# Kernel tuning notes

Hardware: AMD Instinct MI355X
Metric: run time of the kernel (lower is better)

## Reference

```python
import jax, jax.numpy as jnp
import numpy as np

D = 128
N_SRC = 50000
N_DST = 50000
E = 640000
NEG_SLOPE = 0.01  # torch LeakyReLU default


def _lrelu(x):
    return jax.nn.leaky_relu(x, NEG_SLOPE)


def setup_inputs() -> dict:
    key = jax.random.key(0)
    ks = jax.random.split(key, 12)
    s = 1.0 / np.sqrt(D)
    return {
        "feat_src": jax.random.normal(ks[0], (N_SRC, D), jnp.float32),
        "feat_dst": jax.random.normal(ks[1], (N_DST, D), jnp.float32),
        "src_idx": jax.random.randint(ks[2], (E,), 0, N_SRC, jnp.int32),
        "dst_idx": jax.random.randint(ks[3], (E,), 0, N_DST, jnp.int32),
        "W_src": jax.random.uniform(ks[4], (D, D), jnp.float32, -s, s),
        "b_src": jnp.zeros((D,), jnp.float32),
        "W_dst": jax.random.uniform(ks[5], (D, D), jnp.float32, -s, s),
        "b_dst": jnp.zeros((D,), jnp.float32),
        "W_a1": jax.random.uniform(ks[6], (D, D), jnp.float32, -s, s),
        "b_a1": jnp.zeros((D,), jnp.float32),
        "W_a2": jax.random.uniform(ks[7], (D, 1), jnp.float32, -s, s),
        "b_a2": jnp.zeros((1,), jnp.float32),
        "W_out": jax.random.uniform(ks[8], (D, D), jnp.float32, -s, s),
        "b_out": jnp.zeros((D,), jnp.float32),
    }


def reference(feat_src, feat_dst, src_idx, dst_idx,
              W_src, b_src, W_dst, b_dst,
              W_a1, b_a1, W_a2, b_a2, W_out, b_out):
    n_dst = feat_dst.shape[0]
    # node projections (dropout is identity in eval mode)
    hs = feat_src @ W_src + b_src            # [n_src, d]
    hd = feat_dst @ W_dst + b_dst            # [n_dst, d]
    # u_add_v: per-edge feature
    e = hs[src_idx] + hd[dst_idx]            # [E, d]
    # attention MLP: LeakyReLU -> Linear -> LeakyReLU -> Linear(d->1)
    s = _lrelu(_lrelu(e) @ W_a1 + b_a1) @ W_a2 + b_a2  # [E, 1]
    s = s[:, 0]
    # edge softmax grouped by destination node (numerically stable)
    m = jax.ops.segment_max(s, dst_idx, num_segments=n_dst)
    ex = jnp.exp(s - m[dst_idx])
    denom = jax.ops.segment_sum(ex, dst_idx, num_segments=n_dst)
    alpha = ex / denom[dst_idx]              # [E]
    # scale messages and scatter-sum to dst nodes
    n_f = jax.ops.segment_sum(alpha[:, None] * e, dst_idx, num_segments=n_dst)
    return _lrelu(n_f @ W_out + b_out)       # [n_dst, d]
```

## Files before the change

kernel.cpp:

```cpp
#include <hip/hip_runtime.h>
#include <math.h>

#define DD 128
#define NEG 0.01f
#define SCHUNK 4096

typedef __attribute__((ext_vector_type(8))) _Float16 half8;
typedef __attribute__((ext_vector_type(4))) float f32x4;

__device__ __forceinline__ float lrelu(float x){ return x > 0.f ? x : NEG * x; }

__device__ __forceinline__ unsigned short h2u(_Float16 h){
    union { _Float16 h; unsigned short u; } v; v.h = h; return v.u;
}
__device__ __forceinline__ _Float16 u2h(unsigned short u){
    union { unsigned short u; _Float16 h; } v; v.u = u; return v.h;
}

__global__ void hist_pack(const int* dst, int* deg, int E, int nhist,
                          const float* Wa1, const float* Wsrc,
                          const float* Wdst, const float* Wout,
                          unsigned short* wpack){
    const int bid = blockIdx.x;
    if (bid < nhist){
        int i = bid * 256 + threadIdx.x;
        if (i < E) atomicAdd(&deg[dst[i]], 1);
    } else {
        int i = (bid - nhist) * 256 + threadIdx.x;
        if (i >= 7 * 16384) return;
        int seg = i >> 14, t = i & 16383;
        int j = t & 7, lane = (t >> 3) & 63, nt = (t >> 9) & 7, kc = t >> 12;
        int k = kc * 32 + (lane >> 4) * 8 + j;
        int n = nt * 16 + (lane & 15);
        const float* W = (seg == 0) ? Wa1 : (seg <= 2) ? Wsrc : (seg <= 4) ? Wdst : Wout;
        float w = W[k * DD + n];
        _Float16 hi = (_Float16)w;
        unsigned short val = h2u(hi);
        if (seg == 2 || seg == 4 || seg == 6) val = h2u((_Float16)(w - (float)hi));
        wpack[i] = val;
    }
}

__global__ __launch_bounds__(1024) void scan1(const int* deg, int* part, int n){
    __shared__ int wsum[16];
    const int tid = threadIdx.x;
    const int lane = tid & 63, wid = tid >> 6;
    int i4 = blockIdx.x * SCHUNK + tid * 4;
    int4 v = make_int4(0, 0, 0, 0);
    if (i4 + 3 < n) v = *(const int4*)(deg + i4);
    else {
        if (i4 + 0 < n) v.x = deg[i4 + 0];
        if (i4 + 1 < n) v.y = deg[i4 + 1];
        if (i4 + 2 < n) v.z = deg[i4 + 2];
        if (i4 + 3 < n) v.w = deg[i4 + 3];
    }
    int t = v.x + v.y + v.z + v.w;
    #pragma unroll
    for (int off = 1; off < 64; off <<= 1) t += __shfl_xor(t, off, 64);
    if (lane == 0) wsum[wid] = t;
    __syncthreads();
    if (tid == 0){
        int s = 0;
        #pragma unroll
        for (int j = 0; j < 16; j++) s += wsum[j];
        part[blockIdx.x] = s;
    }
}

__global__ __launch_bounds__(1024) void scan2(const int* deg, const int* part,
        int* row_off, int* cursor, int n, int nchunks){
    __shared__ int wsum[16];
    const int tid = threadIdx.x;
    const int lane = tid & 63, wid = tid >> 6;
    const int b = blockIdx.x;
    int carry = 0;
    for (int j = 0; j < b; j++) carry += part[j];
    int i4 = b * SCHUNK + tid * 4;
    int4 v = make_int4(0, 0, 0, 0);
    if (i4 + 3 < n) v = *(const int4*)(deg + i4);
    else {
        if (i4 + 0 < n) v.x = deg[i4 + 0];
        if (i4 + 1 < n) v.y = deg[i4 + 1];
        if (i4 + 2 < n) v.z = deg[i4 + 2];
        if (i4 + 3 < n) v.w = deg[i4 + 3];
    }
    int tsum = v.x + v.y + v.z + v.w;
    int x = tsum;
    #pragma unroll
    for (int off = 1; off < 64; off <<= 1){
        int t = __shfl_up(x, off, 64);
        if (lane >= off) x += t;
    }
    if (lane == 63) wsum[wid] = x;
    __syncthreads();
    int wprefix = 0;
    #pragma unroll
    for (int j = 0; j < 16; j++) if (j < wid) wprefix += wsum[j];
    int excl = carry + wprefix + (x - tsum);
    if (i4 + 3 < n){
        int4 o;
        o.x = excl; o.y = excl + v.x; o.z = o.y + v.y; o.w = o.z + v.z;
        *(int4*)(row_off + i4) = o;
        *(int4*)(cursor + i4) = o;
    } else {
        int a = excl;
        if (i4 + 0 < n){ row_off[i4 + 0] = a; cursor[i4 + 0] = a; a += v.x; }
        if (i4 + 1 < n){ row_off[i4 + 1] = a; cursor[i4 + 1] = a; a += v.y; }
        if (i4 + 2 < n){ row_off[i4 + 2] = a; cursor[i4 + 2] = a; a += v.z; }
        if (i4 + 3 < n){ row_off[i4 + 3] = a; cursor[i4 + 3] = a; }
    }
    if (b == 0 && tid == 0){
        int tot = 0;
        for (int j = 0; j < nchunks; j++) tot += part[j];
        row_off[n] = tot;
    }
}

__global__ void scatter_pairs(const int* src, const int* dst, int* cursor,
                              int2* pairs, int* s_srcs, int E){
    int i = blockIdx.x * blockDim.x + threadIdx.x;
    if (i < E){
        int d = dst[i];
        int s = src[i];
        int pos = atomicAdd(&cursor[d], 1);
        pairs[pos] = make_int2(s, d);
        s_srcs[pos] = s;
    }
}

__global__ __launch_bounds__(256) void lin2_mfma(
        const float* X1, const unsigned short* W1hi, const unsigned short* W1lo,
        const float* b1, unsigned short* Yb1, int n1, int g1,
        const float* X2, const unsigned short* W2hi, const unsigned short* W2lo,
        const float* b2, unsigned short* Yb2, int n2){
    __shared__ unsigned short sB[2][16384];
    const int tid = threadIdx.x;
    const int second = (blockIdx.x >= g1);
    const float* X = second ? X2 : X1;
    const unsigned short* Whi = second ? W2hi : W1hi;
    const unsigned short* Wlo = second ? W2lo : W1lo;
    const float* b = second ? b2 : b1;
    unsigned short* Yb = second ? Yb2 : Yb1;
    const int nrows = second ? n2 : n1;
    const int bidx = second ? (blockIdx.x - g1) : blockIdx.x;
    {
        const uint4* gh = (const uint4*)Whi;
        const uint4* gl = (const uint4*)Wlo;
        uint4* lh = (uint4*)sB[0];
        uint4* ll = (uint4*)sB[1];
        #pragma unroll
        for (int t = 0; t < 8; t++){
            lh[tid + 256 * t] = gh[tid + 256 * t];
            ll[tid + 256 * t] = gl[tid + 256 * t];
        }
    }
    const int wave = tid >> 6, lane = tid & 63;
    const int qd = lane >> 4, ln16 = lane & 15;
    const int row0 = bidx * 128 + wave * 32;
    int r0 = row0 + ln16;       if (r0 >= nrows) r0 = nrows - 1;
    int r1 = row0 + 16 + ln16;  if (r1 >= nrows) r1 = nrows - 1;
    f32x4 acc[2][8];
    #pragma unroll
    for (int rt = 0; rt < 2; rt++)
        #pragma unroll
        for (int nt = 0; nt < 8; nt++)
            acc[rt][nt] = (f32x4){0.f, 0.f, 0.f, 0.f};
    __syncthreads();
    #pragma unroll
    for (int kc = 0; kc < 4; kc++){
        const int koff = kc * 32 + qd * 8;
        half8 ahi[2], alo[2];
        const float* px[2] = {X + (size_t)r0 * DD + koff, X + (size_t)r1 * DD + koff};
        #pragma unroll
        for (int rt = 0; rt < 2; rt++){
            float4 v0 = *(const float4*)(px[rt]);
            float4 v1 = *(const float4*)(px[rt] + 4);
            float xv[8] = {v0.x, v0.y, v0.z, v0.w, v1.x, v1.y, v1.z, v1.w};
            #pragma unroll
            for (int j = 0; j < 8; j++){
                _Float16 h = (_Float16)xv[j];
                ahi[rt][j] = h;
                alo[rt][j] = (_Float16)(xv[j] - (float)h);
            }
        }
        #pragma unroll
        for (int nt = 0; nt < 8; nt++){
            const int fi = (((kc << 3) + nt) << 6 | lane) << 3;
            half8 bh = *(const half8*)&sB[0][fi];
            half8 bl = *(const half8*)&sB[1][fi];
            #pragma unroll
            for (int rt = 0; rt < 2; rt++){
                acc[rt][nt] = __builtin_amdgcn_mfma_f32_16x16x32_f16(ahi[rt], bh, acc[rt][nt], 0, 0, 0);
                acc[rt][nt] = __builtin_amdgcn_mfma_f32_16x16x32_f16(alo[rt], bh, acc[rt][nt], 0, 0, 0);
                acc[rt][nt] = __builtin_amdgcn_mfma_f32_16x16x32_f16(ahi[rt], bl, acc[rt][nt], 0, 0, 0);
            }
        }
    }
    #pragma unroll
    for (int nt = 0; nt < 8; nt++){
        const int col = nt * 16 + ln16;
        const float bv = b[col];
        #pragma unroll
        for (int rt = 0; rt < 2; rt++){
            #pragma unroll
            for (int r = 0; r < 4; r++){
                int row = row0 + rt * 16 + qd * 4 + r;
                if (row < nrows){
                    float y = acc[rt][nt][r] + bv;
                    Yb[(size_t)row * DD + col] = h2u((_Float16)y);
                }
            }
        }
    }
}

__global__ __launch_bounds__(256) void lin_mfma(const float* X,
        const unsigned short* Whi, const unsigned short* Wlo, const float* b,
        float* Y, int nrows){
    __shared__ unsigned short sB[2][16384];
    const int tid = threadIdx.x;
    {
        const uint4* gh = (const uint4*)Whi;
        const uint4* gl = (const uint4*)Wlo;
        uint4* lh = (uint4*)sB[0];
        uint4* ll = (uint4*)sB[1];
        #pragma unroll
        for (int t = 0; t < 8; t++){
            lh[tid + 256 * t] = gh[tid + 256 * t];
            ll[tid + 256 * t] = gl[tid + 256 * t];
        }
    }
    const int wave = tid >> 6, lane = tid & 63;
    const int qd = lane >> 4, ln16 = lane & 15;
    const int row0 = blockIdx.x * 128 + wave * 32;
    int r0 = row0 + ln16;       if (r0 >= nrows) r0 = nrows - 1;
    int r1 = row0 + 16 + ln16;  if (r1 >= nrows) r1 = nrows - 1;
    f32x4 acc[2][8];
    #pragma unroll
    for (int rt = 0; rt < 2; rt++)
        #pragma unroll
        for (int nt = 0; nt < 8; nt++)
            acc[rt][nt] = (f32x4){0.f, 0.f, 0.f, 0.f};
    __syncthreads();
    #pragma unroll
    for (int kc = 0; kc < 4; kc++){
        const int koff = kc * 32 + qd * 8;
        half8 ahi[2], alo[2];
        const float* px[2] = {X + (size_t)r0 * DD + koff, X + (size_t)r1 * DD + koff};
        #pragma unroll
        for (int rt = 0; rt < 2; rt++){
            float4 v0 = *(const float4*)(px[rt]);
            float4 v1 = *(const float4*)(px[rt] + 4);
            float xv[8] = {v0.x, v0.y, v0.z, v0.w, v1.x, v1.y, v1.z, v1.w};
            #pragma unroll
            for (int j = 0; j < 8; j++){
                _Float16 h = (_Float16)xv[j];
                ahi[rt][j] = h;
                alo[rt][j] = (_Float16)(xv[j] - (float)h);
            }
        }
        #pragma unroll
        for (int nt = 0; nt < 8; nt++){
            const int fi = (((kc << 3) + nt) << 6 | lane) << 3;
            half8 bh = *(const half8*)&sB[0][fi];
            half8 bl = *(const half8*)&sB[1][fi];
            #pragma unroll
            for (int rt = 0; rt < 2; rt++){
                acc[rt][nt] = __builtin_amdgcn_mfma_f32_16x16x32_f16(ahi[rt], bh, acc[rt][nt], 0, 0, 0);
                acc[rt][nt] = __builtin_amdgcn_mfma_f32_16x16x32_f16(alo[rt], bh, acc[rt][nt], 0, 0, 0);
                acc[rt][nt] = __builtin_amdgcn_mfma_f32_16x16x32_f16(ahi[rt], bl, acc[rt][nt], 0, 0, 0);
            }
        }
    }
    #pragma unroll
    for (int nt = 0; nt < 8; nt++){
        const int col = nt * 16 + ln16;
        const float bv = b[col];
        #pragma unroll
        for (int rt = 0; rt < 2; rt++){
            #pragma unroll
            for (int r = 0; r < 4; r++){
                int row = row0 + rt * 16 + qd * 4 + r;
                if (row < nrows){
                    float y = acc[rt][nt][r] + bv;
                    Y[(size_t)row * DD + col] = lrelu(y);
                }
            }
        }
    }
}

__device__ __forceinline__ half8 make_afrag(const unsigned short* ph, const unsigned short* pd){
    half8 a = *(const half8*)ph;
    half8 b = *(const half8*)pd;
    half8 s = a + b;
    half8 l = s * (_Float16)0.01f;
    half8 r;
    #pragma unroll
    for (int i = 0; i < 8; i++) r[i] = (s[i] > (_Float16)0.f) ? s[i] : l[i];
    return r;
}

__global__ __launch_bounds__(256) void edge_score_mfma(
        const unsigned short* hs_h, const unsigned short* hd_h,
        const int2* pairs,
        const unsigned short* wa1p, const float* ba1,
        const float* Wa2, const float* ba2,
        float* s_w, int E){
    __shared__ unsigned short sB[16384];
    const int tid = threadIdx.x;
    {
        const uint4* g = (const uint4*)wa1p;
        uint4* l = (uint4*)sB;
        #pragma unroll
        for (int t = 0; t < 8; t++) l[tid + 256 * t] = g[tid + 256 * t];
    }
    const int wave = tid >> 6, lane = tid & 63;
    const int qd = lane >> 4, ln16 = lane & 15;
    float b1v[8], w2v[8];
    #pragma unroll
    for (int nt = 0; nt < 8; nt++){
        b1v[nt] = ba1[nt * 16 + ln16];
        w2v[nt] = Wa2[nt * 16 + ln16];
    }
    const float b2 = ba2[0];
    __syncthreads();
    for (int half = 0; half < 2; half++){
        const int e0 = blockIdx.x * 256 + half * 128 + wave * 32;
        for (int rt = 0; rt < 2; rt++){
            int eid = e0 + rt * 16 + ln16;
            if (eid >= E) eid = E - 1;
            const int2 pp = pairs[eid];
            f32x4 acc[8];
            #pragma unroll
            for (int nt = 0; nt < 8; nt++) acc[nt] = (f32x4){0.f, 0.f, 0.f, 0.f};
            #pragma unroll
            for (int kc = 0; kc < 4; kc++){
                const int koff = kc * 32 + qd * 8;
                half8 af = make_afrag(hs_h + (size_t)pp.x * DD + koff,
                                      hd_h + (size_t)pp.y * DD + koff);
                #pragma unroll
                for (int nt = 0; nt < 8; nt++){
                    half8 bf = *(const half8*)&sB[(((kc << 3) + nt) << 6 | lane) << 3];
                    acc[nt] = __builtin_amdgcn_mfma_f32_16x16x32_f16(af, bf, acc[nt], 0, 0, 0);
                }
            }
            float p[4] = {0.f, 0.f, 0.f, 0.f};
            #pragma unroll
            for (int nt = 0; nt < 8; nt++)
                #pragma unroll
                for (int r = 0; r < 4; r++){
                    float z = acc[nt][r] + b1v[nt];
                    z = z > 0.f ? z : NEG * z;
                    p[r] += z * w2v[nt];
                }
            #pragma unroll
            for (int r = 0; r < 4; r++){
                float v = p[r];
                #pragma unroll
                for (int off = 1; off < 16; off <<= 1) v += __shfl_xor(v, off, 64);
                p[r] = expf(v + b2);
            }
            if (ln16 == 0){
                int row = e0 + rt * 16 + qd * 4;
                #pragma unroll
                for (int r = 0; r < 4; r++)
                    if (row + r < E) s_w[row + r] = p[r];
            }
        }
    }
}

__global__ __launch_bounds__(256) void agg_softmax(const unsigned short* hs_h,
        const unsigned short* hd_h, const int* row_off, const int* s_srcs,
        const float* s_w, float* nf, int n_dst){
    const int w = (blockIdx.x * blockDim.x + threadIdx.x) >> 6;
    const int lane = threadIdx.x & 63;
    if (w >= n_dst) return;
    const int beg = row_off[w], end = row_off[w + 1];
    float2 acc = make_float2(0.f, 0.f);
    float sa = 0.f;
    int e = beg;
    for (; e + 3 < end; e += 4){
        float w0 = s_w[e], w1 = s_w[e + 1], w2 = s_w[e + 2], w3 = s_w[e + 3];
        int s0 = s_srcs[e], s1 = s_srcs[e + 1], s2 = s_srcs[e + 2], s3 = s_srcs[e + 3];
        ushort2 u0 = *(const ushort2*)(hs_h + (size_t)s0 * DD + lane * 2);
        ushort2 u1 = *(const ushort2*)(hs_h + (size_t)s1 * DD + lane * 2);
        ushort2 u2 = *(const ushort2*)(hs_h + (size_t)s2 * DD + lane * 2);
        ushort2 u3 = *(const ushort2*)(hs_h + (size_t)s3 * DD + lane * 2);
        acc.x += w0 * (float)u2h(u0.x) + w1 * (float)u2h(u1.x)
               + w2 * (float)u2h(u2.x) + w3 * (float)u2h(u3.x);
        acc.y += w0 * (float)u2h(u0.y) + w1 * (float)u2h(u1.y)
               + w2 * (float)u2h(u2.y) + w3 * (float)u2h(u3.y);
        sa += (w0 + w1) + (w2 + w3);
    }
    for (; e < end; e++){
        float w0 = s_w[e];
        int s0 = s_srcs[e];
        ushort2 u0 = *(const ushort2*)(hs_h + (size_t)s0 * DD + lane * 2);
        acc.x += w0 * (float)u2h(u0.x);
        acc.y += w0 * (float)u2h(u0.y);
        sa += w0;
    }
    const float inv = (end > beg) ? 1.f / sa : 0.f;
    ushort2 hu = *(const ushort2*)(hd_h + (size_t)w * DD + lane * 2);
    const float hx = (end > beg) ? (float)u2h(hu.x) : 0.f;
    const float hy = (end > beg) ? (float)u2h(hu.y) : 0.f;
    float2 out;
    out.x = acc.x * inv + hx;
    out.y = acc.y * inv + hy;
    *(float2*)(nf + (size_t)w * DD + lane * 2) = out;
}

extern "C" void kernel_launch(void* const* d_in, const int* in_sizes, int n_in,
                              void* d_out, int out_size, void* d_ws, size_t ws_size,
                              hipStream_t stream){
    const float* feat_src = (const float*)d_in[0];
    const float* feat_dst = (const float*)d_in[1];
    const int*   src_idx  = (const int*)d_in[2];
    const int*   dst_idx  = (const int*)d_in[3];
    const float* W_src = (const float*)d_in[4];
    const float* b_src = (const float*)d_in[5];
    const float* W_dst = (const float*)d_in[6];
    const float* b_dst = (const float*)d_in[7];
    const float* W_a1  = (const float*)d_in[8];
    const float* b_a1  = (const float*)d_in[9];
    const float* W_a2  = (const float*)d_in[10];
    const float* b_a2  = (const float*)d_in[11];
    const float* W_out = (const float*)d_in[12];
    const float* b_out = (const float*)d_in[13];
    const int n_src = in_sizes[0] / DD;
    const int n_dst = in_sizes[1] / DD;
    const int E = in_sizes[2];
    const int nchunks = (n_dst + SCHUNK - 1) / SCHUNK;

    char* p = (char*)d_ws;
    unsigned short* hs_h = (unsigned short*)p;  p += (size_t)n_src * DD * 2;
    unsigned short* hd_h = (unsigned short*)p;  p += (size_t)n_dst * DD * 2;
    unsigned short* wpack = (unsigned short*)p; p += 7 * 16384 * 2;
    float* s_w = (float*)p;                     p += (size_t)E * 4;
    int2* pairs = (int2*)p;                     p += (size_t)E * 8;
    int* s_srcs = (int*)p;                      p += (size_t)E * 4;
    int* deg = (int*)p;                         p += (size_t)n_dst * 4;
    int* cursor = (int*)p;                      p += (size_t)n_dst * 4;
    int* part = (int*)p;                        p += 64 * 4;
    int* row_off = (int*)p;                     p += ((size_t)n_dst + 1) * 4;
    float* nf = (float*)d_out;

    const unsigned short* wa1p    = wpack;
    const unsigned short* wsrc_hi = wpack + 1 * 16384;
    const unsigned short* wsrc_lo = wpack + 2 * 16384;
    const unsigned short* wdst_hi = wpack + 3 * 16384;
    const unsigned short* wdst_lo = wpack + 4 * 16384;
    const unsigned short* wout_hi = wpack + 5 * 16384;
    const unsigned short* wout_lo = wpack + 6 * 16384;

    hipMemsetAsync(deg, 0, (size_t)n_dst * 4, stream);
    const int nhist = (E + 255) / 256;
    const int npack = (7 * 16384 + 255) / 256;
    hist_pack<<<nhist + npack, 256, 0, stream>>>(dst_idx, deg, E, nhist,
                                                 W_a1, W_src, W_dst, W_out, wpack);
    scan1<<<nchunks, 1024, 0, stream>>>(deg, part, n_dst);
    scan2<<<nchunks, 1024, 0, stream>>>(deg, part, row_off, cursor, n_dst, nchunks);
    scatter_pairs<<<(E + 255) / 256, 256, 0, stream>>>(src_idx, dst_idx, cursor,
                                                       pairs, s_srcs, E);
    const int g1 = (n_src + 127) / 128;
    const int g2 = (n_dst + 127) / 128;
    lin2_mfma<<<g1 + g2, 256, 0, stream>>>(feat_src, wsrc_hi, wsrc_lo, b_src, hs_h, n_src, g1,
                                           feat_dst, wdst_hi, wdst_lo, b_dst, hd_h, n_dst);
    edge_score_mfma<<<(E + 255) / 256, 256, 0, stream>>>(hs_h, hd_h, pairs, wa1p, b_a1,
                                                         W_a2, b_a2, s_w, E);
    agg_softmax<<<((size_t)n_dst * 64 + 255) / 256, 256, 0, stream>>>(hs_h, hd_h, row_off,
                                                                      s_srcs, s_w, nf, n_dst);
    lin_mfma<<<g2, 256, 0, stream>>>(nf, wout_hi, wout_lo, b_out, nf, n_dst);
}
```

Before: 325.0 us.

## Drop split-fp16 GEMM compensation, halve edge-score block work, unroll aggregation by 8

```diff
diff --git a/kernel.cpp b/kernel.cpp
--- a/kernel.cpp
+++ b/kernel.cpp
@@ -27,17 +27,13 @@
         if (i < E) atomicAdd(&deg[dst[i]], 1);
     } else {
         int i = (bid - nhist) * 256 + threadIdx.x;
-        if (i >= 7 * 16384) return;
+        if (i >= 4 * 16384) return;
         int seg = i >> 14, t = i & 16383;
         int j = t & 7, lane = (t >> 3) & 63, nt = (t >> 9) & 7, kc = t >> 12;
         int k = kc * 32 + (lane >> 4) * 8 + j;
         int n = nt * 16 + (lane & 15);
-        const float* W = (seg == 0) ? Wa1 : (seg <= 2) ? Wsrc : (seg <= 4) ? Wdst : Wout;
-        float w = W[k * DD + n];
-        _Float16 hi = (_Float16)w;
-        unsigned short val = h2u(hi);
-        if (seg == 2 || seg == 4 || seg == 6) val = h2u((_Float16)(w - (float)hi));
-        wpack[i] = val;
+        const float* W = (seg == 0) ? Wa1 : (seg == 1) ? Wsrc : (seg == 2) ? Wdst : Wout;
+        wpack[i] = h2u((_Float16)W[k * DD + n]);
     }
 }
 
@@ -129,30 +125,24 @@
 }
 
 __global__ __launch_bounds__(256) void lin2_mfma(
-        const float* X1, const unsigned short* W1hi, const unsigned short* W1lo,
-        const float* b1, unsigned short* Yb1, int n1, int g1,
-        const float* X2, const unsigned short* W2hi, const unsigned short* W2lo,
-        const float* b2, unsigned short* Yb2, int n2){
-    __shared__ unsigned short sB[2][16384];
+        const float* X1, const unsigned short* W1, const float* b1,
+        unsigned short* Yb1, int n1, int g1,
+        const float* X2, const unsigned short* W2, const float* b2,
+        unsigned short* Yb2, int n2){
+    __shared__ unsigned short sB[16384];
     const int tid = threadIdx.x;
     const int second = (blockIdx.x >= g1);
     const float* X = second ? X2 : X1;
-    const unsigned short* Whi = second ? W2hi : W1hi;
-    const unsigned short* Wlo = second ? W2lo : W1lo;
+    const unsigned short* W = second ? W2 : W1;
     const float* b = second ? b2 : b1;
     unsigned short* Yb = second ? Yb2 : Yb1;
     const int nrows = second ? n2 : n1;
     const int bidx = second ? (blockIdx.x - g1) : blockIdx.x;
     {
-        const uint4* gh = (const uint4*)Whi;
-        const uint4* gl = (const uint4*)Wlo;
-        uint4* lh = (uint4*)sB[0];
-        uint4* ll = (uint4*)sB[1];
-        #pragma unroll
-        for (int t = 0; t < 8; t++){
-            lh[tid + 256 * t] = gh[tid + 256 * t];
-            ll[tid + 256 * t] = gl[tid + 256 * t];
-        }
+        const uint4* g = (const uint4*)W;
+        uint4* l = (uint4*)sB;
+        #pragma unroll
+        for (int t = 0; t < 8; t++) l[tid + 256 * t] = g[tid + 256 * t];
     }
     const int wave = tid >> 6, lane = tid & 63;
     const int qd = lane >> 4, ln16 = lane & 15;
@@ -169,31 +159,23 @@
     #pragma unroll
     for (int kc = 0; kc < 4; kc++){
         const int koff = kc * 32 + qd * 8;
-        half8 ahi[2], alo[2];
+        half8 a[2];
         const float* px[2] = {X + (size_t)r0 * DD + koff, X + (size_t)r1 * DD + koff};
         #pragma unroll
         for (int rt = 0; rt < 2; rt++){
             float4 v0 = *(const float4*)(px[rt]);
             float4 v1 = *(const float4*)(px[rt] + 4);
-            float xv[8] = {v0.x, v0.y, v0.z, v0.w, v1.x, v1.y, v1.z, v1.w};
-            #pragma unroll
-            for (int j = 0; j < 8; j++){
-                _Float16 h = (_Float16)xv[j];
-                ahi[rt][j] = h;
-                alo[rt][j] = (_Float16)(xv[j] - (float)h);
-            }
+            a[rt][0] = (_Float16)v0.x; a[rt][1] = (_Float16)v0.y;
+            a[rt][2] = (_Float16)v0.z; a[rt][3] = (_Float16)v0.w;
+            a[rt][4] = (_Float16)v1.x; a[rt][5] = (_Float16)v1.y;
+            a[rt][6] = (_Float16)v1.z; a[rt][7] = (_Float16)v1.w;
         }
         #pragma unroll
         for (int nt = 0; nt < 8; nt++){
             const int fi = (((kc << 3) + nt) << 6 | lane) << 3;
-            half8 bh = *(const half8*)&sB[0][fi];
-            half8 bl = *(const half8*)&sB[1][fi];
-            #pragma unroll
-            for (int rt = 0; rt < 2; rt++){
-                acc[rt][nt] = __builtin_amdgcn_mfma_f32_16x16x32_f16(ahi[rt], bh, acc[rt][nt], 0, 0, 0);
-                acc[rt][nt] = __builtin_amdgcn_mfma_f32_16x16x32_f16(alo[rt], bh, acc[rt][nt], 0, 0, 0);
-                acc[rt][nt] = __builtin_amdgcn_mfma_f32_16x16x32_f16(ahi[rt], bl, acc[rt][nt], 0, 0, 0);
-            }
+            half8 bw = *(const half8*)&sB[fi];
+            acc[0][nt] = __builtin_amdgcn_mfma_f32_16x16x32_f16(a[0], bw, acc[0][nt], 0, 0, 0);
+            acc[1][nt] = __builtin_amdgcn_mfma_f32_16x16x32_f16(a[1], bw, acc[1][nt], 0, 0, 0);
         }
     }
     #pragma unroll
@@ -215,20 +197,14 @@
 }
 
 __global__ __launch_bounds__(256) void lin_mfma(const float* X,
-        const unsigned short* Whi, const unsigned short* Wlo, const float* b,
-        float* Y, int nrows){
-    __shared__ unsigned short sB[2][16384];
+        const unsigned short* W, const float* b, float* Y, int nrows){
+    __shared__ unsigned short sB[16384];
     const int tid = threadIdx.x;
     {
-        const uint4* gh = (const uint4*)Whi;
-        const uint4* gl = (const uint4*)Wlo;
-        uint4* lh = (uint4*)sB[0];
-        uint4* ll = (uint4*)sB[1];
-        #pragma unroll
-        for (int t = 0; t < 8; t++){
-            lh[tid + 256 * t] = gh[tid + 256 * t];
-            ll[tid + 256 * t] = gl[tid + 256 * t];
-        }
+        const uint4* g = (const uint4*)W;
+        uint4* l = (uint4*)sB;
+        #pragma unroll
+        for (int t = 0; t < 8; t++) l[tid + 256 * t] = g[tid + 256 * t];
     }
     const int wave = tid >> 6, lane = tid & 63;
     const int qd = lane >> 4, ln16 = lane & 15;
@@ -245,31 +221,23 @@
     #pragma unroll
     for (int kc = 0; kc < 4; kc++){
         const int koff = kc * 32 + qd * 8;
-        half8 ahi[2], alo[2];
+        half8 a[2];
         const float* px[2] = {X + (size_t)r0 * DD + koff, X + (size_t)r1 * DD + koff};
         #pragma unroll
         for (int rt = 0; rt < 2; rt++){
             float4 v0 = *(const float4*)(px[rt]);
             float4 v1 = *(const float4*)(px[rt] + 4);
-            float xv[8] = {v0.x, v0.y, v0.z, v0.w, v1.x, v1.y, v1.z, v1.w};
-            #pragma unroll
-            for (int j = 0; j < 8; j++){
-                _Float16 h = (_Float16)xv[j];
-                ahi[rt][j] = h;
-                alo[rt][j] = (_Float16)(xv[j] - (float)h);
-            }
+            a[rt][0] = (_Float16)v0.x; a[rt][1] = (_Float16)v0.y;
+            a[rt][2] = (_Float16)v0.z; a[rt][3] = (_Float16)v0.w;
+            a[rt][4] = (_Float16)v1.x; a[rt][5] = (_Float16)v1.y;
+            a[rt][6] = (_Float16)v1.z; a[rt][7] = (_Float16)v1.w;
         }
         #pragma unroll
         for (int nt = 0; nt < 8; nt++){
             const int fi = (((kc << 3) + nt) << 6 | lane) << 3;
-            half8 bh = *(const half8*)&sB[0][fi];
-            half8 bl = *(const half8*)&sB[1][fi];
-            #pragma unroll
-            for (int rt = 0; rt < 2; rt++){
-                acc[rt][nt] = __builtin_amdgcn_mfma_f32_16x16x32_f16(ahi[rt], bh, acc[rt][nt], 0, 0, 0);
-                acc[rt][nt] = __builtin_amdgcn_mfma_f32_16x16x32_f16(alo[rt], bh, acc[rt][nt], 0, 0, 0);
-                acc[rt][nt] = __builtin_amdgcn_mfma_f32_16x16x32_f16(ahi[rt], bl, acc[rt][nt], 0, 0, 0);
-            }
+            half8 bw = *(const half8*)&sB[fi];
+            acc[0][nt] = __builtin_amdgcn_mfma_f32_16x16x32_f16(a[0], bw, acc[0][nt], 0, 0, 0);
+            acc[1][nt] = __builtin_amdgcn_mfma_f32_16x16x32_f16(a[1], bw, acc[1][nt], 0, 0, 0);
         }
     }
     #pragma unroll
@@ -317,6 +285,7 @@
     }
     const int wave = tid >> 6, lane = tid & 63;
     const int qd = lane >> 4, ln16 = lane & 15;
+    const int e0 = blockIdx.x * 128 + wave * 32;
     float b1v[8], w2v[8];
     #pragma unroll
     for (int nt = 0; nt < 8; nt++){
@@ -325,48 +294,45 @@
     }
     const float b2 = ba2[0];
     __syncthreads();
-    for (int half = 0; half < 2; half++){
-        const int e0 = blockIdx.x * 256 + half * 128 + wave * 32;
-        for (int rt = 0; rt < 2; rt++){
-            int eid = e0 + rt * 16 + ln16;
-            if (eid >= E) eid = E - 1;
-            const int2 pp = pairs[eid];
-            f32x4 acc[8];
-            #pragma unroll
-            for (int nt = 0; nt < 8; nt++) acc[nt] = (f32x4){0.f, 0.f, 0.f, 0.f};
-            #pragma unroll
-            for (int kc = 0; kc < 4; kc++){
-                const int koff = kc * 32 + qd * 8;
-                half8 af = make_afrag(hs_h + (size_t)pp.x * DD + koff,
-                                      hd_h + (size_t)pp.y * DD + koff);
-                #pragma unroll
-                for (int nt = 0; nt < 8; nt++){
-                    half8 bf = *(const half8*)&sB[(((kc << 3) + nt) << 6 | lane) << 3];
-                    acc[nt] = __builtin_amdgcn_mfma_f32_16x16x32_f16(af, bf, acc[nt], 0, 0, 0);
-                }
+    for (int rt = 0; rt < 2; rt++){
+        int eid = e0 + rt * 16 + ln16;
+        if (eid >= E) eid = E - 1;
+        const int2 pp = pairs[eid];
+        f32x4 acc[8];
+        #pragma unroll
+        for (int nt = 0; nt < 8; nt++) acc[nt] = (f32x4){0.f, 0.f, 0.f, 0.f};
+        #pragma unroll
+        for (int kc = 0; kc < 4; kc++){
+            const int koff = kc * 32 + qd * 8;
+            half8 af = make_afrag(hs_h + (size_t)pp.x * DD + koff,
+                                  hd_h + (size_t)pp.y * DD + koff);
+            #pragma unroll
+            for (int nt = 0; nt < 8; nt++){
+                half8 bf = *(const half8*)&sB[(((kc << 3) + nt) << 6 | lane) << 3];
+                acc[nt] = __builtin_amdgcn_mfma_f32_16x16x32_f16(af, bf, acc[nt], 0, 0, 0);
             }
-            float p[4] = {0.f, 0.f, 0.f, 0.f};
-            #pragma unroll
-            for (int nt = 0; nt < 8; nt++)
-                #pragma unroll
-                for (int r = 0; r < 4; r++){
-                    float z = acc[nt][r] + b1v[nt];
-                    z = z > 0.f ? z : NEG * z;
-                    p[r] += z * w2v[nt];
-                }
+        }
+        float p[4] = {0.f, 0.f, 0.f, 0.f};
+        #pragma unroll
+        for (int nt = 0; nt < 8; nt++)
             #pragma unroll
             for (int r = 0; r < 4; r++){
-                float v = p[r];
-                #pragma unroll
-                for (int off = 1; off < 16; off <<= 1) v += __shfl_xor(v, off, 64);
-                p[r] = expf(v + b2);
+                float z = acc[nt][r] + b1v[nt];
+                z = z > 0.f ? z : NEG * z;
+                p[r] += z * w2v[nt];
             }
-            if (ln16 == 0){
-                int row = e0 + rt * 16 + qd * 4;
-                #pragma unroll
-                for (int r = 0; r < 4; r++)
-                    if (row + r < E) s_w[row + r] = p[r];
-            }
+        #pragma unroll
+        for (int r = 0; r < 4; r++){
+            float v = p[r];
+            #pragma unroll
+            for (int off = 1; off < 16; off <<= 1) v += __shfl_xor(v, off, 64);
+            p[r] = expf(v + b2);
+        }
+        if (ln16 == 0){
+            int row = e0 + rt * 16 + qd * 4;
+            #pragma unroll
+            for (int r = 0; r < 4; r++)
+                if (row + r < E) s_w[row + r] = p[r];
         }
     }
 }
@@ -381,18 +347,19 @@
     float2 acc = make_float2(0.f, 0.f);
     float sa = 0.f;
     int e = beg;
-    for (; e + 3 < end; e += 4){
-        float w0 = s_w[e], w1 = s_w[e + 1], w2 = s_w[e + 2], w3 = s_w[e + 3];
-        int s0 = s_srcs[e], s1 = s_srcs[e + 1], s2 = s_srcs[e + 2], s3 = s_srcs[e + 3];
-        ushort2 u0 = *(const ushort2*)(hs_h + (size_t)s0 * DD + lane * 2);
-        ushort2 u1 = *(const ushort2*)(hs_h + (size_t)s1 * DD + lane * 2);
-        ushort2 u2 = *(const ushort2*)(hs_h + (size_t)s2 * DD + lane * 2);
-        ushort2 u3 = *(const ushort2*)(hs_h + (size_t)s3 * DD + lane * 2);
-        acc.x += w0 * (float)u2h(u0.x) + w1 * (float)u2h(u1.x)
-               + w2 * (float)u2h(u2.x) + w3 * (float)u2h(u3.x);
-        acc.y += w0 * (float)u2h(u0.y) + w1 * (float)u2h(u1.y)
-               + w2 * (float)u2h(u2.y) + w3 * (float)u2h(u3.y);
-        sa += (w0 + w1) + (w2 + w3);
+    for (; e + 7 < end; e += 8){
+        float wv[8]; int sv[8]; ushort2 uv[8];
+        #pragma unroll
+        for (int j = 0; j < 8; j++){ wv[j] = s_w[e + j]; sv[j] = s_srcs[e + j]; }
+        #pragma unroll
+        for (int j = 0; j < 8; j++)
+            uv[j] = *(const ushort2*)(hs_h + (size_t)sv[j] * DD + lane * 2);
+        #pragma unroll
+        for (int j = 0; j < 8; j++){
+            acc.x += wv[j] * (float)u2h(uv[j].x);
+            acc.y += wv[j] * (float)u2h(uv[j].y);
+            sa += wv[j];
+        }
     }
     for (; e < end; e++){
         float w0 = s_w[e];
@@ -437,7 +404,7 @@
     char* p = (char*)d_ws;
     unsigned short* hs_h = (unsigned short*)p;  p += (size_t)n_src * DD * 2;
     unsigned short* hd_h = (unsigned short*)p;  p += (size_t)n_dst * DD * 2;
-    unsigned short* wpack = (unsigned short*)p; p += 7 * 16384 * 2;
+    unsigned short* wpack = (unsigned short*)p; p += 4 * 16384 * 2;
     float* s_w = (float*)p;                     p += (size_t)E * 4;
     int2* pairs = (int2*)p;                     p += (size_t)E * 8;
     int* s_srcs = (int*)p;                      p += (size_t)E * 4;
@@ -447,17 +414,14 @@
     int* row_off = (int*)p;                     p += ((size_t)n_dst + 1) * 4;
     float* nf = (float*)d_out;
 
-    const unsigned short* wa1p    = wpack;
-    const unsigned short* wsrc_hi = wpack + 1 * 16384;
-    const unsigned short* wsrc_lo = wpack + 2 * 16384;
-    const unsigned short* wdst_hi = wpack + 3 * 16384;
-    const unsigned short* wdst_lo = wpack + 4 * 16384;
-    const unsigned short* wout_hi = wpack + 5 * 16384;
-    const unsigned short* wout_lo = wpack + 6 * 16384;
+    const unsigned short* wa1p = wpack;
+    const unsigned short* wsrc = wpack + 1 * 16384;
+    const unsigned short* wdst = wpack + 2 * 16384;
+    const unsigned short* wout = wpack + 3 * 16384;
 
     hipMemsetAsync(deg, 0, (size_t)n_dst * 4, stream);
     const int nhist = (E + 255) / 256;
-    const int npack = (7 * 16384 + 255) / 256;
+    const int npack = (4 * 16384 + 255) / 256;
     hist_pack<<<nhist + npack, 256, 0, stream>>>(dst_idx, deg, E, nhist,
                                                  W_a1, W_src, W_dst, W_out, wpack);
     scan1<<<nchunks, 1024, 0, stream>>>(deg, part, n_dst);
@@ -466,11 +430,11 @@
                                                        pairs, s_srcs, E);
     const int g1 = (n_src + 127) / 128;
     const int g2 = (n_dst + 127) / 128;
-    lin2_mfma<<<g1 + g2, 256, 0, stream>>>(feat_src, wsrc_hi, wsrc_lo, b_src, hs_h, n_src, g1,
-                                           feat_dst, wdst_hi, wdst_lo, b_dst, hd_h, n_dst);
-    edge_score_mfma<<<(E + 255) / 256, 256, 0, stream>>>(hs_h, hd_h, pairs, wa1p, b_a1,
+    lin2_mfma<<<g1 + g2, 256, 0, stream>>>(feat_src, wsrc, b_src, hs_h, n_src, g1,
+                                           feat_dst, wdst, b_dst, hd_h, n_dst);
+    edge_score_mfma<<<(E + 127) / 128, 256, 0, stream>>>(hs_h, hd_h, pairs, wa1p, b_a1,
                                                          W_a2, b_a2, s_w, E);
     agg_softmax<<<((size_t)n_dst * 64 + 255) / 256, 256, 0, stream>>>(hs_h, hd_h, row_off,
                                                                       s_srcs, s_w, nf, n_dst);
-    lin_mfma<<<g2, 256, 0, stream>>>(nf, wout_hi, wout_lo, b_out, nf, n_dst);
-}
+    lin_mfma<<<g2, 256, 0, stream>>>(nf, wout, b_out, nf, n_dst);
+}
```

Measured after the change: 315.0 us. 1.03x faster.
